# Kernel tuning notes

Measured on AMD Instinct MI355X. Metric: run time of the kernel, lower is better.

The kernel has to match this reference:

```python
import jax, jax.numpy as jnp
import numpy as np


def setup_inputs() -> dict:
    key = jax.random.key(0)
    ks = jax.random.split(key, 8)
    B, T, D, H = 4, 4096, 1024, 64
    scale = D ** -0.5
    return {
        "x": jax.random.normal(ks[0], (B, T, D), dtype=jnp.float32),
        "mask": jax.random.randint(ks[1], (B, T), 0, 2, dtype=jnp.int32),
        "wq": jax.random.normal(ks[2], (H, D), dtype=jnp.float32) * scale,
        "bq": jax.random.normal(ks[3], (H,), dtype=jnp.float32) * 0.02,
        "wk": jax.random.normal(ks[4], (H, D), dtype=jnp.float32) * scale,
        "bk": jax.random.normal(ks[5], (H,), dtype=jnp.float32) * 0.02,
        "wv": jax.random.normal(ks[6], (H, D), dtype=jnp.float32) * scale,
        "bv": jax.random.normal(ks[7], (H,), dtype=jnp.float32) * 0.02,
    }


def reference(x, mask, wq, bq, wk, bk, wv, bv):
    # x: [B,T,D]; wq/wk/wv: [H,D] (torch Linear convention), mask: [B,T] int
    head_size = wq.shape[0]
    q = jnp.einsum("btd,hd->bth", x, wq) + bq  # [B,T,H]
    k = jnp.einsum("btd,hd->bth", x, wk) + bk
    v = jnp.einsum("btd,hd->bth", x, wv) + bv
    attn = jnp.einsum("bth,bsh->bts", q, k) * (head_size ** -0.5)  # [B,T,T]
    pad_mask = mask.astype(bool)[:, None, :]  # [B,1,T], True = keep
    attn = jnp.where(pad_mask, attn, jnp.float32(-1e9))
    attn = jax.nn.softmax(attn, axis=-1)
    # dropout is identity in eval/deterministic mode
    return jnp.einsum("bts,bsh->bth", attn, v)  # [B,T,H]
```

## Files before the change

kernel.cpp:

```cpp
#include <hip/hip_runtime.h>
#include <math.h>

#define BATCH 4
#define SEQ   4096
#define DIM   1024
#define HEAD  64
#define MROWS (BATCH*SEQ)
#define KT    64
#define QBLK  64

typedef __attribute__((ext_vector_type(8))) short short8;
typedef __attribute__((ext_vector_type(4))) float f32x4;

static __device__ __forceinline__ unsigned short f2b(float f) {
    union { float f; unsigned u; } v; v.f = f;
    return (unsigned short)((v.u + 0x7FFFu + ((v.u >> 16) & 1u)) >> 16);
}
static __device__ __forceinline__ unsigned cvtpk(float a, float b) {
    unsigned r;
    asm("v_cvt_pk_bf16_f32 %0, %1, %2" : "=v"(r) : "v"(a), "v"(b));
    return r;
}
static __device__ __forceinline__ void lds_barrier() {
    asm volatile("s_waitcnt lgkmcnt(0)" ::: "memory");
    __builtin_amdgcn_s_barrier();
}

#define QSC (0.125f * 1.4426950408889634f)
__global__ __launch_bounds__(256) void wconv_kernel(
    const float* __restrict__ wq, const float* __restrict__ bq,
    const float* __restrict__ wk, const float* __restrict__ bk,
    const float* __restrict__ wv, const float* __restrict__ bv,
    unsigned short* __restrict__ Wb, float* __restrict__ biasAll)
{
    int idx = blockIdx.x * 256 + threadIdx.x;
    int e   = idx * 4;
    int row = e >> 10;
    int col = e & 1023;
    const float* src = (row < 64) ? wq : (row < 128) ? wk : wv;
    float s = (row < 64) ? QSC : 1.0f;
    float4 g = *(const float4*)&src[(size_t)(row & 63) * DIM + col];
    ushort4 o;
    o.x = f2b(g.x * s); o.y = f2b(g.y * s); o.z = f2b(g.z * s); o.w = f2b(g.w * s);
    *(ushort4*)&Wb[e] = o;
    if (idx < 192) {
        const float* bs = (idx < 64) ? bq : (idx < 128) ? bk : bv;
        biasAll[idx] = bs[idx & 63] * ((idx < 64) ? QSC : 1.0f);
    }
}

#define NIT (DIM / 32)
__global__ __launch_bounds__(256) void qkvmm_kernel(
    const float* __restrict__ x, const unsigned short* __restrict__ Wb,
    const float* __restrict__ biasAll,
    unsigned short* __restrict__ qout, unsigned short* __restrict__ kout,
    unsigned short* __restrict__ vtout)
{
    __shared__ unsigned short xs[2][32 * 32];
    __shared__ unsigned short ws[2][192 * 32];

    const int tid  = threadIdx.x;
    const int m0   = blockIdx.x * 32;
    const int bb   = m0 >> 12;
    const int lane = tid & 63;
    const int w    = tid >> 6;
    const int lr   = lane & 15;
    const int lg   = lane >> 4;
    const int mrow  = (w >> 1) * 16;
    const int nbase = (w & 1) * 6;

    const int sxrow = tid >> 2, sxlg = tid & 3;
    int wn[3], wlg[3];
    #pragma unroll
    for (int i = 0; i < 3; ++i) { int idx = tid + i * 256; wn[i] = idx >> 2; wlg[i] = idx & 3; }

    f32x4 acc[6];
    #pragma unroll
    for (int nt = 0; nt < 6; ++nt) acc[nt] = (f32x4){0.f, 0.f, 0.f, 0.f};

    float4 xg0[3], xg1[3];
    short8 wg0[3], wg1[3], wg2[3];

    auto LOADR = [&](int ko, int s) {
        if (tid < 128) {
            const float* xp = &x[(size_t)(m0 + sxrow) * DIM + ko + sxlg * 8];
            xg0[s] = *(const float4*)xp;
            xg1[s] = *(const float4*)(xp + 4);
        }
        wg0[s] = *(const short8*)&Wb[(size_t)wn[0] * DIM + ko + wlg[0] * 8];
        wg1[s] = *(const short8*)&Wb[(size_t)wn[1] * DIM + ko + wlg[1] * 8];
        wg2[s] = *(const short8*)&Wb[(size_t)wn[2] * DIM + ko + wlg[2] * 8];
    };
    auto WRITE = [&](int buf, int s) {
        if (tid < 128) {
            uint4 c;
            c.x = cvtpk(xg0[s].x, xg0[s].y); c.y = cvtpk(xg0[s].z, xg0[s].w);
            c.z = cvtpk(xg1[s].x, xg1[s].y); c.w = cvtpk(xg1[s].z, xg1[s].w);
            *(uint4*)&xs[buf][sxrow * 32 + ((sxlg * 8) ^ ((sxrow & 3) * 8))] = c;
        }
        *(short8*)&ws[buf][wn[0] * 32 + ((wlg[0] * 8) ^ ((wn[0] & 3) * 8))] = wg0[s];
        *(short8*)&ws[buf][wn[1] * 32 + ((wlg[1] * 8) ^ ((wn[1] & 3) * 8))] = wg1[s];
        *(short8*)&ws[buf][wn[2] * 32 + ((wlg[2] * 8) ^ ((wn[2] & 3) * 8))] = wg2[s];
    };

    LOADR(0, 0); LOADR(32, 1); LOADR(64, 2);
    WRITE(0, 0);
    lds_barrier();

    #pragma unroll
    for (int it = 0; it < NIT; ++it) {
        const int cur = it & 1;
        if (it + 3 < NIT) LOADR((it + 3) * 32, (it + 3) % 3);
        if (it + 1 < NIT) WRITE(cur ^ 1, (it + 1) % 3);

        const int arow = mrow + lr;
        short8 af = *(const short8*)&xs[cur][arow * 32 + ((lg * 8) ^ ((arow & 3) * 8))];
        #pragma unroll
        for (int nt = 0; nt < 6; ++nt) {
            int n = (nbase + nt) * 16 + lr;
            short8 bf = *(const short8*)&ws[cur][n * 32 + ((lg * 8) ^ ((n & 3) * 8))];
            acc[nt] = __builtin_amdgcn_mfma_f32_16x16x32_bf16(af, bf, acc[nt], 0, 0, 0);
        }
        lds_barrier();
    }

    #pragma unroll
    for (int nt = 0; nt < 6; ++nt) {
        int gn = (nbase + nt) * 16 + lr;
        float bv_ = biasAll[gn];
        #pragma unroll
        for (int r = 0; r < 4; ++r) {
            int grow = m0 + mrow + lg * 4 + r;
            unsigned short val = f2b(acc[nt][r] + bv_);
            if (gn < 64)       qout[(size_t)grow * HEAD + gn] = val;
            else if (gn < 128) kout[(size_t)grow * HEAD + gn - 64] = val;
            else {
                int t = (m0 & 4095) + mrow + lg * 4 + r;
                vtout[((size_t)bb * HEAD + gn - 128) * SEQ + t] = val;
            }
        }
    }
}

__global__ __launch_bounds__(256, 4) void flashmm_kernel(
    const unsigned short* __restrict__ qb, const unsigned short* __restrict__ kb,
    const unsigned short* __restrict__ vt, const int* __restrict__ mask,
    float* __restrict__ opart, float* __restrict__ mpart, float* __restrict__ lpart,
    int nsplit)
{
    const int b  = blockIdx.y;
    const int t0 = blockIdx.x * QBLK;
    const int z  = blockIdx.z;
    const int tid  = threadIdx.x;
    const int lane = tid & 63;
    const int w    = tid >> 6;
    const int lr = lane & 15;
    const int lg = lane >> 4;
    const int span = SEQ / nsplit;
    const int s_begin = z * span, s_end = s_begin + span;

    __shared__ unsigned short ks_l[KT * HEAD];
    __shared__ unsigned short vt_l[HEAD * KT];
    __shared__ unsigned short ps_l[4][16 * KT];
    __shared__ float mkf[KT];

    const unsigned short* qrow = qb + ((size_t)(b * SEQ + t0 + w * 16 + lr)) * HEAD;
    const short8 qf0 = *(const short8*)(qrow + lg * 8);
    const short8 qf1 = *(const short8*)(qrow + 32 + lg * 8);

    f32x4 acc_o[4];
    #pragma unroll
    for (int nt = 0; nt < 4; ++nt) acc_o[nt] = (f32x4){0.f, 0.f, 0.f, 0.f};
    float m_r = -INFINITY, l_r = 0.f;

    short8 kg[2], vg[2];
    float mgf = 0.f;

    auto LOADR = [&](int st) {
        #pragma unroll
        for (int i = 0; i < 2; ++i) {
            int c   = tid + i * 256;
            int row = c >> 3;
            int h0  = (c & 7) * 8;
            kg[i] = *(const short8*)(kb + ((size_t)(b * SEQ + st + row)) * HEAD + h0);
            vg[i] = *(const short8*)(vt + ((size_t)(b * HEAD + row)) * SEQ + st + h0);
        }
        if (tid < KT) mgf = (mask[(size_t)b * SEQ + st + tid] != 0) ? 0.f : -1e9f;
    };
    auto WRITE = [&]() {
        #pragma unroll
        for (int i = 0; i < 2; ++i) {
            int c   = tid + i * 256;
            int row = c >> 3;
            int h0  = (c & 7) * 8;
            *(short8*)&ks_l[row * HEAD + (h0 ^ ((row & 7) << 3))] = kg[i];
            *(short8*)&vt_l[row * KT + (h0 ^ ((row & 7) << 3))] = vg[i];
        }
        if (tid < KT) mkf[tid] = mgf;
    };

    LOADR(s_begin);
    for (int st = s_begin; st < s_end; st += KT) {
        __syncthreads();
        WRITE();
        __syncthreads();
        if (st + KT < s_end) LOADR(st + KT);

        f32x4 sT[4];
        __builtin_amdgcn_s_setprio(1);
        #pragma unroll
        for (int ct = 0; ct < 4; ++ct) {
            int krow = ct * 16 + lr;
            short8 kf0 = *(const short8*)&ks_l[krow * HEAD + ((lg * 8) ^ ((krow & 7) << 3))];
            short8 kf1 = *(const short8*)&ks_l[krow * HEAD + ((32 + lg * 8) ^ ((krow & 7) << 3))];
            f32x4 zz = (f32x4){0.f, 0.f, 0.f, 0.f};
            zz = __builtin_amdgcn_mfma_f32_16x16x32_bf16(kf0, qf0, zz, 0, 0, 0);
            zz = __builtin_amdgcn_mfma_f32_16x16x32_bf16(kf1, qf1, zz, 0, 0, 0);
            sT[ct] = zz;
        }
        __builtin_amdgcn_s_setprio(0);

        #pragma unroll
        for (int ct = 0; ct < 4; ++ct) {
            f32x4 mb = *(const f32x4*)&mkf[ct * 16 + lg * 4];
            sT[ct][0] += mb[0]; sT[ct][1] += mb[1];
            sT[ct][2] += mb[2]; sT[ct][3] += mb[3];
        }

        float mx = sT[0][0];
        #pragma unroll
        for (int ct = 0; ct < 4; ++ct)
            #pragma unroll
            for (int r = 0; r < 4; ++r) mx = fmaxf(mx, sT[ct][r]);
        mx = fmaxf(mx, __shfl_xor(mx, 16));
        mx = fmaxf(mx, __shfl_xor(mx, 32));

        bool defer = __all(mx <= m_r + 8.f);
        float base = defer ? m_r : fmaxf(m_r, mx);

        float rs = 0.f;
        #pragma unroll
        for (int ct = 0; ct < 4; ++ct)
            #pragma unroll
            for (int r = 0; r < 4; ++r) {
                float p = __builtin_amdgcn_exp2f(sT[ct][r] - base);
                sT[ct][r] = p;
                rs += p;
            }
        rs += __shfl_xor(rs, 16);
        rs += __shfl_xor(rs, 32);

        if (defer) {
            l_r += rs;
        } else {
            float sf = __builtin_amdgcn_exp2f(m_r - base);
            l_r = l_r * sf + rs;
            m_r = base;
            #pragma unroll
            for (int r = 0; r < 4; ++r) {
                float sfr = __shfl(sf, lg * 4 + r);
                #pragma unroll
                for (int nt = 0; nt < 4; ++nt) acc_o[nt][r] *= sfr;
            }
        }

        #pragma unroll
        for (int ct = 0; ct < 4; ++ct) {
            uint2 pk;
            pk.x = cvtpk(sT[ct][0], sT[ct][1]);
            pk.y = cvtpk(sT[ct][2], sT[ct][3]);
            *(uint2*)&ps_l[w][lr * KT + ((ct * 16 + lg * 4) ^ ((lr & 7) << 3))] = pk;
        }

        __builtin_amdgcn_s_setprio(1);
        #pragma unroll
        for (int kk = 0; kk < 2; ++kk) {
            int s0 = kk * 32 + lg * 8;
            short8 pf = *(const short8*)&ps_l[w][lr * KT + (s0 ^ ((lr & 7) << 3))];
            #pragma unroll
            for (int nt = 0; nt < 4; ++nt) {
                int hrow = nt * 16 + lr;
                short8 vf = *(const short8*)&vt_l[hrow * KT + (s0 ^ ((hrow & 7) << 3))];
                acc_o[nt] = __builtin_amdgcn_mfma_f32_16x16x32_bf16(pf, vf, acc_o[nt], 0, 0, 0);
            }
        }
        __builtin_amdgcn_s_setprio(0);
    }

    const size_t rbase = (size_t)z * MROWS + (size_t)b * SEQ + t0 + w * 16;
    const size_t obase = rbase * HEAD;
    #pragma unroll
    for (int nt = 0; nt < 4; ++nt)
        #pragma unroll
        for (int r = 0; r < 4; ++r) {
            int R = lg * 4 + r;
            opart[obase + (size_t)R * HEAD + nt * 16 + lr] = acc_o[nt][r];
        }
    if (lg == 0) {
        mpart[rbase + lr] = m_r;
        lpart[rbase + lr] = l_r;
    }
}

__global__ __launch_bounds__(256) void combine_kernel(
    const float* __restrict__ op, const float* __restrict__ mp,
    const float* __restrict__ lp, float* __restrict__ out, int nsplit)
{
    int idx = blockIdx.x * 256 + threadIdx.x;
    int row = idx >> 4;
    int h4  = (idx & 15) * 4;
    float mstar = -INFINITY;
    for (int s = 0; s < nsplit; ++s)
        mstar = fmaxf(mstar, mp[(size_t)s * MROWS + row]);
    float L = 0.f;
    float ax = 0.f, ay = 0.f, az = 0.f, aw = 0.f;
    for (int s = 0; s < nsplit; ++s) {
        float wgt = __builtin_amdgcn_exp2f(mp[(size_t)s * MROWS + row] - mstar);
        L += lp[(size_t)s * MROWS + row] * wgt;
        float4 o = *(const float4*)&op[((size_t)s * MROWS + row) * HEAD + h4];
        ax += o.x * wgt; ay += o.y * wgt; az += o.z * wgt; aw += o.w * wgt;
    }
    float r = 1.f / L;
    float4 res; res.x = ax * r; res.y = ay * r; res.z = az * r; res.w = aw * r;
    *(float4*)&out[(size_t)row * HEAD + h4] = res;
}

extern "C" void kernel_launch(void* const* d_in, const int* in_sizes, int n_in,
                              void* d_out, int out_size, void* d_ws, size_t ws_size,
                              hipStream_t stream) {
    const float* x    = (const float*)d_in[0];
    const int*   mask = (const int*)d_in[1];
    const float* wq   = (const float*)d_in[2];
    const float* bq   = (const float*)d_in[3];
    const float* wk   = (const float*)d_in[4];
    const float* bk   = (const float*)d_in[5];
    const float* wv   = (const float*)d_in[6];
    const float* bv   = (const float*)d_in[7];
    float* out = (float*)d_out;
    (void)in_sizes; (void)n_in; (void)out_size;

    const size_t NB = (size_t)MROWS * HEAD;
    unsigned short* qw  = (unsigned short*)d_ws;
    unsigned short* kw  = qw + NB;
    unsigned short* vtw = kw + NB;
    unsigned short* Wb  = vtw + NB;
    float* biasAll = (float*)(Wb + (size_t)192 * DIM);
    float* mpart   = biasAll + 192;

    const size_t base = 3 * NB * 2 + (size_t)192 * DIM * 2 + 192 * 4;
    const size_t per  = (size_t)MROWS * 8 + NB * 4;
    int KS = 1;
    if      (ws_size >= base + 4 * per) KS = 4;
    else if (ws_size >= base + 2 * per) KS = 2;

    float* lpart = mpart + (size_t)KS * MROWS;
    float* opart = lpart + (size_t)KS * MROWS;

    wconv_kernel<<<dim3(192), 256, 0, stream>>>(wq, bq, wk, bk, wv, bv, Wb, biasAll);
    qkvmm_kernel<<<dim3(MROWS / 32), 256, 0, stream>>>(x, Wb, biasAll, qw, kw, vtw);
    flashmm_kernel<<<dim3(SEQ / QBLK, BATCH, KS), 256, 0, stream>>>(qw, kw, vtw, mask,
                                                                    opart, mpart, lpart, KS);
    combine_kernel<<<dim3(MROWS * 16 / 256), 256, 0, stream>>>(opart, mpart, lpart, out, KS);
}
```

Before: 71.48 us.

## Split QKV projection over K dimension with fp32 partials and a reduce kernel

The QKV projection GEMM is split along the reduction dimension into 2 or 4 chunks via a second grid axis, and each block writes fp32 partial sums to workspace. A new reduce kernel sums the partials, adds bias, converts to bf16 and scatters to q, k and transposed v. The goal is more blocks in flight to fill the GPU on the 512-block projection. The cost is extra fp32 partial traffic of several MB plus one more kernel launch. The partial buffer reuses the flash-attention workspace region, and flash attention is now fixed at KS=4 with no workspace-size check.

```diff
diff --git a/kernel.cpp b/kernel.cpp
--- a/kernel.cpp
+++ b/kernel.cpp
@@ -6,6 +6,7 @@
 #define DIM   1024
 #define HEAD  64
 #define MROWS (BATCH*SEQ)
+#define NCOL  192
 #define KT    64
 #define QBLK  64
 
@@ -49,19 +50,17 @@
     }
 }
 
-#define NIT (DIM / 32)
-__global__ __launch_bounds__(256) void qkvmm_kernel(
+template<int NITS>
+__global__ __launch_bounds__(256) void qkvsplit_kernel(
     const float* __restrict__ x, const unsigned short* __restrict__ Wb,
-    const float* __restrict__ biasAll,
-    unsigned short* __restrict__ qout, unsigned short* __restrict__ kout,
-    unsigned short* __restrict__ vtout)
+    float* __restrict__ partQ)
 {
     __shared__ unsigned short xs[2][32 * 32];
-    __shared__ unsigned short ws[2][192 * 32];
+    __shared__ unsigned short ws[2][NCOL * 32];
 
     const int tid  = threadIdx.x;
     const int m0   = blockIdx.x * 32;
-    const int bb   = m0 >> 12;
+    const int ko0  = blockIdx.y * (NITS * 32);
     const int lane = tid & 63;
     const int w    = tid >> 6;
     const int lr   = lane & 15;
@@ -103,15 +102,15 @@
         *(short8*)&ws[buf][wn[2] * 32 + ((wlg[2] * 8) ^ ((wn[2] & 3) * 8))] = wg2[s];
     };
 
-    LOADR(0, 0); LOADR(32, 1); LOADR(64, 2);
+    LOADR(ko0, 0); LOADR(ko0 + 32, 1); LOADR(ko0 + 64, 2);
     WRITE(0, 0);
     lds_barrier();
 
     #pragma unroll
-    for (int it = 0; it < NIT; ++it) {
+    for (int it = 0; it < NITS; ++it) {
         const int cur = it & 1;
-        if (it + 3 < NIT) LOADR((it + 3) * 32, (it + 3) % 3);
-        if (it + 1 < NIT) WRITE(cur ^ 1, (it + 1) % 3);
+        if (it + 3 < NITS) LOADR(ko0 + (it + 3) * 32, (it + 3) % 3);
+        if (it + 1 < NITS) WRITE(cur ^ 1, (it + 1) % 3);
 
         const int arow = mrow + lr;
         short8 af = *(const short8*)&xs[cur][arow * 32 + ((lg * 8) ^ ((arow & 3) * 8))];
@@ -124,21 +123,44 @@
         lds_barrier();
     }
 
+    float* dst = partQ + (size_t)blockIdx.y * MROWS * NCOL;
     #pragma unroll
     for (int nt = 0; nt < 6; ++nt) {
         int gn = (nbase + nt) * 16 + lr;
-        float bv_ = biasAll[gn];
         #pragma unroll
         for (int r = 0; r < 4; ++r) {
             int grow = m0 + mrow + lg * 4 + r;
-            unsigned short val = f2b(acc[nt][r] + bv_);
-            if (gn < 64)       qout[(size_t)grow * HEAD + gn] = val;
-            else if (gn < 128) kout[(size_t)grow * HEAD + gn - 64] = val;
-            else {
-                int t = (m0 & 4095) + mrow + lg * 4 + r;
-                vtout[((size_t)bb * HEAD + gn - 128) * SEQ + t] = val;
-            }
-        }
+            dst[(size_t)grow * NCOL + gn] = acc[nt][r];
+        }
+    }
+}
+
+__global__ __launch_bounds__(256) void qkvreduce_kernel(
+    const float* __restrict__ partQ, const float* __restrict__ biasAll,
+    unsigned short* __restrict__ qout, unsigned short* __restrict__ kout,
+    unsigned short* __restrict__ vtout, int ksq)
+{
+    int idx  = blockIdx.x * 256 + threadIdx.x;
+    int col  = idx % NCOL;
+    int row0 = (idx / NCOL) * 4;
+    float s0 = 0.f, s1 = 0.f, s2 = 0.f, s3 = 0.f;
+    for (int ks = 0; ks < ksq; ++ks) {
+        const float* p = partQ + ((size_t)ks * MROWS + row0) * NCOL + col;
+        s0 += p[0]; s1 += p[NCOL]; s2 += p[2 * NCOL]; s3 += p[3 * NCOL];
+    }
+    float bv = biasAll[col];
+    unsigned short v0 = f2b(s0 + bv), v1 = f2b(s1 + bv);
+    unsigned short v2 = f2b(s2 + bv), v3 = f2b(s3 + bv);
+    if (col < 64) {
+        unsigned short* o = qout + (size_t)row0 * HEAD + col;
+        o[0] = v0; o[HEAD] = v1; o[2 * HEAD] = v2; o[3 * HEAD] = v3;
+    } else if (col < 128) {
+        unsigned short* o = kout + (size_t)row0 * HEAD + (col - 64);
+        o[0] = v0; o[HEAD] = v1; o[2 * HEAD] = v2; o[3 * HEAD] = v3;
+    } else {
+        int bb = row0 >> 12, t = row0 & 4095;
+        unsigned short* o = vtout + ((size_t)bb * HEAD + col - 128) * SEQ + t;
+        o[0] = v0; o[1] = v1; o[2] = v2; o[3] = v3;
     }
 }
 
@@ -344,20 +366,28 @@
     unsigned short* kw  = qw + NB;
     unsigned short* vtw = kw + NB;
     unsigned short* Wb  = vtw + NB;
-    float* biasAll = (float*)(Wb + (size_t)192 * DIM);
-    float* mpart   = biasAll + 192;
-
-    const size_t base = 3 * NB * 2 + (size_t)192 * DIM * 2 + 192 * 4;
-    const size_t per  = (size_t)MROWS * 8 + NB * 4;
-    int KS = 1;
-    if      (ws_size >= base + 4 * per) KS = 4;
-    else if (ws_size >= base + 2 * per) KS = 2;
-
+    float* biasAll = (float*)(Wb + (size_t)NCOL * DIM);
+    float* shared  = biasAll + 192;
+
+    const size_t pre      = 3 * NB * 2 + (size_t)NCOL * DIM * 2 + 192 * 4;
+    const size_t qkvpart4 = (size_t)4 * MROWS * NCOL * 4;
+    const int KS = 4;
+    const size_t flashB   = (size_t)KS * (MROWS * 8 + NB * 4);
+
+    int KSQ = (ws_size >= pre + (qkvpart4 > flashB ? qkvpart4 : flashB)) ? 4 : 2;
+
+    float* partQ = shared;
+    float* mpart = shared;
     float* lpart = mpart + (size_t)KS * MROWS;
     float* opart = lpart + (size_t)KS * MROWS;
 
     wconv_kernel<<<dim3(192), 256, 0, stream>>>(wq, bq, wk, bk, wv, bv, Wb, biasAll);
-    qkvmm_kernel<<<dim3(MROWS / 32), 256, 0, stream>>>(x, Wb, biasAll, qw, kw, vtw);
+    if (KSQ == 4)
+        qkvsplit_kernel<8><<<dim3(MROWS / 32, 4), 256, 0, stream>>>(x, Wb, partQ);
+    else
+        qkvsplit_kernel<16><<<dim3(MROWS / 32, 2), 256, 0, stream>>>(x, Wb, partQ);
+    qkvreduce_kernel<<<dim3(MROWS / 4 * NCOL / 256), 256, 0, stream>>>(
+        partQ, biasAll, qw, kw, vtw, KSQ);
     flashmm_kernel<<<dim3(SEQ / QBLK, BATCH, KS), 256, 0, stream>>>(qw, kw, vtw, mask,
                                                                     opart, mpart, lpart, KS);
     combine_kernel<<<dim3(MROWS * 16 / 256), 256, 0, stream>>>(opart, mpart, lpart, out, KS);
```

After: 84.76 us. 1.19x slower.
